# Kernel tuning notes

Measured on AMD Instinct MI355X. Metric: run time of the kernel, lower is better.

The kernel has to match this reference:

```python
import jax, jax.numpy as jnp
import numpy as np

B, S, D, H, E, K = 2, 1024, 768, 12, 8, 2
DF = 4 * D
HD = D // H
EPS = 1e-5

def layer_norm(x, g, b):
    m = jnp.mean(x, axis=-1, keepdims=True)
    v = jnp.mean(jnp.square(x - m), axis=-1, keepdims=True)
    return (x - m) * jax.lax.rsqrt(v + EPS) * g + b

def setup_inputs() -> dict:
    key = jax.random.key(0)
    ks = jax.random.split(key, 16)
    s = lambda i, shape, sc: jax.random.normal(ks[i], shape, jnp.float32) * sc
    return {
        'x': s(0, (B, S, D), 1.0),
        'ln1_g': jnp.ones((D,), jnp.float32), 'ln1_b': jnp.zeros((D,), jnp.float32),
        'Wq': s(1, (D, D), 0.02), 'Wk': s(2, (D, D), 0.02), 'Wv': s(3, (D, D), 0.02),
        'Wo': s(4, (D, D), 0.02), 'bo': jnp.zeros((D,), jnp.float32),
        'ln2_g': jnp.ones((D,), jnp.float32), 'ln2_b': jnp.zeros((D,), jnp.float32),
        'Wr': s(5, (D, E), 0.02), 'br': jnp.zeros((E,), jnp.float32),
        'W1': s(6, (E, D, DF), 0.02), 'b1': jnp.zeros((E, DF), jnp.float32),
        'W2': s(7, (E, DF, D), 0.02), 'b2': jnp.zeros((E, D), jnp.float32),
    }

def _attn(xn, Wq, Wk, Wv, Wo, bo):
    # xn: [B,S,D]
    q = (xn @ Wq).reshape(B, S, H, HD).transpose(0, 2, 1, 3)
    k = (xn @ Wk).reshape(B, S, H, HD).transpose(0, 2, 1, 3)
    v = (xn @ Wv).reshape(B, S, H, HD).transpose(0, 2, 1, 3)
    scores = jnp.einsum('bhqd,bhkd->bhqk', q, k) / jnp.sqrt(jnp.float32(HD))
    causal = jnp.tril(jnp.ones((S, S), bool))
    scores = jnp.where(causal, scores, jnp.float32(-1e9))
    w = jax.nn.softmax(scores, axis=-1)
    out = jnp.einsum('bhqk,bhkd->bhqd', w, v)
    out = out.transpose(0, 2, 1, 3).reshape(B, S, D)
    return out @ Wo + bo

def _smoe(xn, Wr, br, W1, b1, W2, b2):
    logits = xn @ Wr + br                               # [B,S,E]
    topv, topi = jax.lax.top_k(logits, K)               # [B,S,K]
    gw = jax.nn.softmax(topv, axis=-1)                  # softmax over selected experts
    oh = jax.nn.one_hot(topi, E, dtype=xn.dtype)        # [B,S,K,E]
    gate = jnp.einsum('bske,bsk->bse', oh, gw)          # sparse gate, zeros elsewhere
    h = jax.nn.gelu(jnp.einsum('bsd,edf->bsef', xn, W1) + b1, approximate=False)
    eo = jnp.einsum('bsef,efd->bsed', h, W2) + b2       # [B,S,E,D]
    return jnp.einsum('bsed,bse->bsd', eo, gate)

def reference(x, ln1_g, ln1_b, Wq, Wk, Wv, Wo, bo, ln2_g, ln2_b, Wr, br, W1, b1, W2, b2):
    h = x + _attn(layer_norm(x, ln1_g, ln1_b), Wq, Wk, Wv, Wo, bo)
    out = h + _smoe(layer_norm(h, ln2_g, ln2_b), Wr, br, W1, b1, W2, b2)
    return out
```

## Files before the change

### kernel.cpp

```cpp
#include <hip/hip_runtime.h>

using bf16x8 = __attribute__((ext_vector_type(8))) short;
using f32x4  = __attribute__((ext_vector_type(4))) float;

#define DEV __device__ __forceinline__

DEV short f2bf(float x){
  unsigned u = __float_as_uint(x);
  u += 0x7fffu + ((u >> 16) & 1u);
  return (short)(u >> 16);
}
DEV float bf2f(short h){ return __uint_as_float(((unsigned)(unsigned short)h) << 16); }

#define MFMA16(a,b,c) __builtin_amdgcn_mfma_f32_16x16x32_bf16(a,b,c,0,0,0)

DEV void gl_lds16(const void* g, void* l){
  __builtin_amdgcn_global_load_lds(
      (const __attribute__((address_space(1))) unsigned*)g,
      (__attribute__((address_space(3))) unsigned*)l, 16, 0, 0);
}


__global__ void k_transpose(const float* __restrict__ src, long sbatch,
                            short* __restrict__ dhi, short* __restrict__ dlo, long dbatch,
                            int R, int C){
  __shared__ float tile[32][33];
  const float* s = src + (long)blockIdx.z * sbatch;
  int c0 = blockIdx.x * 32, r0 = blockIdx.y * 32;
  int tx = threadIdx.x & 31, ty = threadIdx.x >> 5;
  #pragma unroll
  for (int i = 0; i < 4; i++)
    tile[ty + 8*i][tx] = s[(long)(r0 + ty + 8*i) * C + c0 + tx];
  __syncthreads();
  #pragma unroll
  for (int i = 0; i < 4; i++){
    int c = c0 + ty + 8*i;
    float v = tile[tx][ty + 8*i];
    short hv = f2bf(v);
    long o = (long)blockIdx.z * dbatch + (long)c * R + r0 + tx;
    dhi[o] = hv;
    if (dlo) dlo[o] = f2bf(v - bf2f(hv));
  }
}

__global__ void k_ln1(const float* __restrict__ x, const float* __restrict__ g,
                      const float* __restrict__ bb,
                      short* __restrict__ xh, short* __restrict__ xl){
  int t = blockIdx.x, tid = threadIdx.x;
  const float* xr = x + (long)t * 768;
  float v[3];
  #pragma unroll
  for (int j = 0; j < 3; j++) v[j] = xr[tid + 256*j];
  float s = v[0]+v[1]+v[2];
  float q = v[0]*v[0]+v[1]*v[1]+v[2]*v[2];
  #pragma unroll
  for (int o = 32; o > 0; o >>= 1){ s += __shfl_down(s,o,64); q += __shfl_down(q,o,64); }
  __shared__ float ss[4], qs[4];
  int w = tid >> 6;
  if ((tid & 63) == 0){ ss[w] = s; qs[w] = q; }
  __syncthreads();
  float St = ss[0]+ss[1]+ss[2]+ss[3], Qt = qs[0]+qs[1]+qs[2]+qs[3];
  float mean = St * (1.f/768.f);
  float var  = Qt * (1.f/768.f) - mean*mean;
  float inv  = 1.f / sqrtf(var + 1e-5f);
  #pragma unroll
  for (int j = 0; j < 3; j++){
    int d = tid + 256*j;
    float xn = (v[j]-mean)*inv*g[d] + bb[d];
    short hv = f2bf(xn);
    xh[(long)t*768 + d] = hv;
    xl[(long)t*768 + d] = f2bf(xn - bf2f(hv));
  }
}

__global__ __launch_bounds__(256,2) void k_qkv(
    const short* __restrict__ Ah, const short* __restrict__ Al,
    const short* __restrict__ Bh, const short* __restrict__ Bl,
    short* __restrict__ qh, short* __restrict__ ql,
    short* __restrict__ kh, short* __restrict__ kl,
    short* __restrict__ vh, short* __restrict__ vl){
  int M0 = blockIdx.x * 128, N0 = blockIdx.y * 128;
  __shared__ __align__(16) short lah[128*32], lal[128*32], lbh[128*32], lbl[128*32];
  int tid = threadIdx.x;
  int w = tid >> 6, lane = tid & 63, l15 = lane & 15, quad = lane >> 4;
  int mbase = (w & 1) * 64, nbase = (w >> 1) * 64;
  f32x4 acc[4][4];
  #pragma unroll
  for (int i = 0; i < 4; i++)
    #pragma unroll
    for (int j = 0; j < 4; j++) acc[i][j] = (f32x4){0.f,0.f,0.f,0.f};
  int sr = w*32 + (lane >> 2);
  int sc = ((lane & 3) ^ (sr & 3)) * 8;
  long gA = (long)(M0 + sr)*768 + sc;
  long gB = (long)(N0 + sr)*768 + sc;
  int swq = (quad ^ (l15 & 3)) * 8;
  for (int k0 = 0; k0 < 768; k0 += 32){
    gl_lds16(Ah + gA + k0,          lah + w*1024);
    gl_lds16(Ah + gA + 16*768 + k0, lah + w*1024 + 512);
    gl_lds16(Al + gA + k0,          lal + w*1024);
    gl_lds16(Al + gA + 16*768 + k0, lal + w*1024 + 512);
    gl_lds16(Bh + gB + k0,          lbh + w*1024);
    gl_lds16(Bh + gB + 16*768 + k0, lbh + w*1024 + 512);
    gl_lds16(Bl + gB + k0,          lbl + w*1024);
    gl_lds16(Bl + gB + 16*768 + k0, lbl + w*1024 + 512);
    __syncthreads();
    bf16x8 afh[4], afl[4];
    #pragma unroll
    for (int mt = 0; mt < 4; mt++){
      afh[mt] = *(const bf16x8*)&lah[(mbase+mt*16+l15)*32 + swq];
      afl[mt] = *(const bf16x8*)&lal[(mbase+mt*16+l15)*32 + swq];
    }
    #pragma unroll
    for (int nt = 0; nt < 4; nt++){
      bf16x8 bfh = *(const bf16x8*)&lbh[(nbase+nt*16+l15)*32 + swq];
      bf16x8 bfl = *(const bf16x8*)&lbl[(nbase+nt*16+l15)*32 + swq];
      #pragma unroll
      for (int mt = 0; mt < 4; mt++){
        acc[mt][nt] = MFMA16(afh[mt], bfh, acc[mt][nt]);
        acc[mt][nt] = MFMA16(afh[mt], bfl, acc[mt][nt]);
        acc[mt][nt] = MFMA16(afl[mt], bfh, acc[mt][nt]);
      }
    }
    __syncthreads();
  }
  #pragma unroll
  for (int mt = 0; mt < 4; mt++){
    #pragma unroll
    for (int nt = 0; nt < 4; nt++){
      #pragma unroll
      for (int rg = 0; rg < 4; rg++){
        int m = M0 + mbase + mt*16 + quad*4 + rg;
        int n = N0 + nbase + nt*16 + l15;
        float vv = acc[mt][nt][rg];
        int bi = m >> 10, si = m & 1023;
        if (n < 768){
          float sv = vv * 0.125f;
          short hv = f2bf(sv);
          int hh = n >> 6, hd = n & 63;
          long o = (((long)(bi*12+hh)*1024) + si)*64 + hd;
          qh[o] = hv; ql[o] = f2bf(sv - bf2f(hv));
        } else if (n < 1536){
          int n2 = n - 768;
          short hv = f2bf(vv);
          int hh = n2 >> 6, hd = n2 & 63;
          long o = (((long)(bi*12+hh)*1024) + si)*64 + hd;
          kh[o] = hv; kl[o] = f2bf(vv - bf2f(hv));
        } else {
          int n2 = n - 1536;
          short hv = f2bf(vv);
          int hh = n2 >> 6, hd = n2 & 63;
          long o = (((long)(bi*12+hh)*64) + hd)*1024 + si;
          vh[o] = hv; vl[o] = f2bf(vv - bf2f(hv));
        }
      }
    }
  }
}

__global__ __launch_bounds__(256,3) void k_attn(
    const short* __restrict__ qh, const short* __restrict__ ql,
    const short* __restrict__ kh, const short* __restrict__ kl,
    const short* __restrict__ vth, const short* __restrict__ vtl,
    float* __restrict__ po, float* __restrict__ pm, float* __restrict__ pl){
  int qt = blockIdx.x >> 1, half = blockIdx.x & 1, bh = blockIdx.y;
  int q0 = qt * 64;
  long base = (long)bh * 1024 * 64;
  int ktb = half ? ((qt + 2) >> 1) : 0;
  int kte = half ? (qt + 1) : ((qt + 2) >> 1);
  __shared__ __align__(16) short skh[64*64], skl[64*64], svh[64*64], svl[64*64];
  __shared__ __align__(16) short sph[4][16*72], spl[4][16*72];
  int tid = threadIdx.x, w = tid >> 6, lane = tid & 63, l15 = lane & 15, quad = lane >> 4;
  bf16x8 qfh[2], qfl[2];
  #pragma unroll
  for (int c = 0; c < 2; c++){
    long qa = base + (long)(q0 + w*16 + l15)*64 + c*32 + quad*8;
    qfh[c] = *(const bf16x8*)(qh + qa);
    qfl[c] = *(const bf16x8*)(ql + qa);
  }
  f32x4 oacc[4];
  #pragma unroll
  for (int i = 0; i < 4; i++) oacc[i] = (f32x4){0.f,0.f,0.f,0.f};
  float m_i[4] = {-1e30f,-1e30f,-1e30f,-1e30f};
  float l_i[4] = {0.f,0.f,0.f,0.f};
  const short* gsrc = (w==0) ? kh : (w==1) ? kl : (w==2) ? vth : vtl;
  short* myb = (w==0) ? skh : (w==1) ? skl : (w==2) ? svh : svl;
  bool isv = (w >= 2);
  int rloc = lane >> 3, pch = lane & 7;
  for (int kt = ktb; kt < kte; kt++){
    #pragma unroll
    for (int j = 0; j < 8; j++){
      int r = j*8 + rloc;
      int c = pch ^ (r & 7);
      long ga = isv ? (base + (long)r*1024 + kt*64 + c*8)
                    : (base + (long)(kt*64 + r)*64 + c*8);
      gl_lds16(gsrc + ga, myb + j*512);
    }
    __syncthreads();
    f32x4 sfr[4];
    #pragma unroll
    for (int nt = 0; nt < 4; nt++){
      f32x4 c = (f32x4){0.f,0.f,0.f,0.f};
      int krow = (nt*16 + l15) * 64;
      #pragma unroll
      for (int ch = 0; ch < 2; ch++){
        int pc = ((ch*4 + quad) ^ (l15 & 7)) * 8;
        bf16x8 kfh = *(const bf16x8*)&skh[krow + pc];
        bf16x8 kfl = *(const bf16x8*)&skl[krow + pc];
        c = MFMA16(qfh[ch], kfh, c);
        c = MFMA16(qfh[ch], kfl, c);
        c = MFMA16(qfl[ch], kfh, c);
      }
      sfr[nt] = c;
    }
    if (kt == qt){
      #pragma unroll
      for (int nt = 0; nt < 4; nt++)
        #pragma unroll
        for (int rg = 0; rg < 4; rg++){
          int kp = nt*16 + l15, qp = w*16 + quad*4 + rg;
          if (kp > qp) sfr[nt][rg] = -1e30f;
        }
    }
    float rmax[4];
    #pragma unroll
    for (int rg = 0; rg < 4; rg++)
      rmax[rg] = fmaxf(fmaxf(sfr[0][rg], sfr[1][rg]), fmaxf(sfr[2][rg], sfr[3][rg]));
    #pragma unroll
    for (int xm = 1; xm < 16; xm <<= 1)
      #pragma unroll
      for (int rg = 0; rg < 4; rg++)
        rmax[rg] = fmaxf(rmax[rg], __shfl_xor(rmax[rg], xm, 64));
    float alpha[4];
    #pragma unroll
    for (int rg = 0; rg < 4; rg++){
      float mn = fmaxf(m_i[rg], rmax[rg]);
      alpha[rg] = expf(m_i[rg] - mn);
      m_i[rg] = mn;
    }
    float rsum[4] = {0.f,0.f,0.f,0.f};
    #pragma unroll
    for (int nt = 0; nt < 4; nt++)
      #pragma unroll
      for (int rg = 0; rg < 4; rg++){
        float p = expf(sfr[nt][rg] - m_i[rg]);
        sfr[nt][rg] = p; rsum[rg] += p;
      }
    #pragma unroll
    for (int xm = 1; xm < 16; xm <<= 1)
      #pragma unroll
      for (int rg = 0; rg < 4; rg++)
        rsum[rg] += __shfl_xor(rsum[rg], xm, 64);
    #pragma unroll
    for (int rg = 0; rg < 4; rg++) l_i[rg] = l_i[rg]*alpha[rg] + rsum[rg];
    #pragma unroll
    for (int hd = 0; hd < 4; hd++)
      #pragma unroll
      for (int rg = 0; rg < 4; rg++) oacc[hd][rg] *= alpha[rg];
    #pragma unroll
    for (int nt = 0; nt < 4; nt++)
      #pragma unroll
      for (int rg = 0; rg < 4; rg++){
        float p = sfr[nt][rg];
        short hv = f2bf(p);
        sph[w][(quad*4+rg)*72 + nt*16 + l15] = hv;
        spl[w][(quad*4+rg)*72 + nt*16 + l15] = f2bf(p - bf2f(hv));
      }
    bf16x8 pfh[2], pfl[2];
    #pragma unroll
    for (int ch = 0; ch < 2; ch++){
      pfh[ch] = *(const bf16x8*)&sph[w][l15*72 + ch*32 + quad*8];
      pfl[ch] = *(const bf16x8*)&spl[w][l15*72 + ch*32 + quad*8];
    }
    #pragma unroll
    for (int hd = 0; hd < 4; hd++){
      int vrow = (hd*16 + l15) * 64;
      #pragma unroll
      for (int ch = 0; ch < 2; ch++){
        int pc = ((ch*4 + quad) ^ (l15 & 7)) * 8;
        bf16x8 vfh = *(const bf16x8*)&svh[vrow + pc];
        bf16x8 vfl = *(const bf16x8*)&svl[vrow + pc];
        oacc[hd] = MFMA16(pfh[ch], vfh, oacc[hd]);
        oacc[hd] = MFMA16(pfh[ch], vfl, oacc[hd]);
        oacc[hd] = MFMA16(pfl[ch], vfh, oacc[hd]);
      }
    }
    __syncthreads();
  }
  long pb = ((long)(half*24 + bh)*1024);
  #pragma unroll
  for (int hdt = 0; hdt < 4; hdt++)
    #pragma unroll
    for (int rg = 0; rg < 4; rg++){
      int qp = q0 + w*16 + quad*4 + rg;
      po[(pb + qp)*64 + hdt*16 + l15] = oacc[hdt][rg];
    }
  if (l15 == 0){
    #pragma unroll
    for (int rg = 0; rg < 4; rg++){
      int qp = q0 + w*16 + quad*4 + rg;
      pm[pb + qp] = m_i[rg];
      pl[pb + qp] = l_i[rg];
    }
  }
}

__global__ void k_attn_combine(const float* __restrict__ po, const float* __restrict__ pm,
                               const float* __restrict__ pl,
                               short* __restrict__ oh, short* __restrict__ ol){
  int bh = blockIdx.y, tid = threadIdx.x;
  int r = blockIdx.x*64 + (tid >> 2);
  int c0 = (tid & 3) * 16;
  long i0 = (long)bh*1024 + r;
  long i1 = (long)(24 + bh)*1024 + r;
  float m0 = pm[i0], m1 = pm[i1], l0 = pl[i0], l1 = pl[i1];
  float m = fmaxf(m0, m1);
  float a0 = expf(m0 - m), a1 = expf(m1 - m);
  float inv = 1.f / (a0*l0 + a1*l1);
  a0 *= inv; a1 *= inv;
  int b = bh / 12, hh = bh % 12;
  long ob = ((long)(b*1024 + r))*768 + hh*64 + c0;
  short hv[16], lv[16];
  #pragma unroll
  for (int j = 0; j < 4; j++){
    float4 o0 = *(const float4*)&po[i0*64 + c0 + j*4];
    float4 o1 = *(const float4*)&po[i1*64 + c0 + j*4];
    float vs[4] = {a0*o0.x + a1*o1.x, a0*o0.y + a1*o1.y,
                   a0*o0.z + a1*o1.z, a0*o0.w + a1*o1.w};
    #pragma unroll
    for (int q = 0; q < 4; q++){
      short h = f2bf(vs[q]);
      hv[j*4+q] = h; lv[j*4+q] = f2bf(vs[q] - bf2f(h));
    }
  }
  *(bf16x8*)(oh + ob)     = *(bf16x8*)&hv[0];
  *(bf16x8*)(oh + ob + 8) = *(bf16x8*)&hv[8];
  *(bf16x8*)(ol + ob)     = *(bf16x8*)&lv[0];
  *(bf16x8*)(ol + ob + 8) = *(bf16x8*)&lv[8];
}

__global__ __launch_bounds__(256,2) void k_wo(
    const short* __restrict__ Ah, const short* __restrict__ Al,
    const short* __restrict__ Bh, const short* __restrict__ Bl,
    const float* __restrict__ x, const float* __restrict__ bo,
    float* __restrict__ hout){
  int M0 = blockIdx.x * 128, N0 = blockIdx.y * 128;
  __shared__ __align__(16) short lah[128*32], lal[128*32], lbh[128*32], lbl[128*32];
  int tid = threadIdx.x;
  int w = tid >> 6, lane = tid & 63, l15 = lane & 15, quad = lane >> 4;
  int mbase = (w & 1) * 64, nbase = (w >> 1) * 64;
  f32x4 acc[4][4];
  #pragma unroll
  for (int i = 0; i < 4; i++)
    #pragma unroll
    for (int j = 0; j < 4; j++) acc[i][j] = (f32x4){0.f,0.f,0.f,0.f};
  int sr = w*32 + (lane >> 2);
  int sc = ((lane & 3) ^ (sr & 3)) * 8;
  long gA = (long)(M0 + sr)*768 + sc;
  long gB = (long)(N0 + sr)*768 + sc;
  int swq = (quad ^ (l15 & 3)) * 8;
  for (int k0 = 0; k0 < 768; k0 += 32){
    gl_lds16(Ah + gA + k0,          lah + w*1024);
    gl_lds16(Ah + gA + 16*768 + k0, lah + w*1024 + 512);
    gl_lds16(Al + gA + k0,          lal + w*1024);
    gl_lds16(Al + gA + 16*768 + k0, lal + w*1024 + 512);
    gl_lds16(Bh + gB + k0,          lbh + w*1024);
    gl_lds16(Bh + gB + 16*768 + k0, lbh + w*1024 + 512);
    gl_lds16(Bl + gB + k0,          lbl + w*1024);
    gl_lds16(Bl + gB + 16*768 + k0, lbl + w*1024 + 512);
    __syncthreads();
    bf16x8 afh[4], afl[4];
    #pragma unroll
    for (int mt = 0; mt < 4; mt++){
      afh[mt] = *(const bf16x8*)&lah[(mbase+mt*16+l15)*32 + swq];
      afl[mt] = *(const bf16x8*)&lal[(mbase+mt*16+l15)*32 + swq];
    }
    #pragma unroll
    for (int nt = 0; nt < 4; nt++){
      bf16x8 bfh = *(const bf16x8*)&lbh[(nbase+nt*16+l15)*32 + swq];
      bf16x8 bfl = *(const bf16x8*)&lbl[(nbase+nt*16+l15)*32 + swq];
      #pragma unroll
      for (int mt = 0; mt < 4; mt++){
        acc[mt][nt] = MFMA16(afh[mt], bfh, acc[mt][nt]);
        acc[mt][nt] = MFMA16(afh[mt], bfl, acc[mt][nt]);
        acc[mt][nt] = MFMA16(afl[mt], bfh, acc[mt][nt]);
      }
    }
    __syncthreads();
  }
  #pragma unroll
  for (int mt = 0; mt < 4; mt++)
    #pragma unroll
    for (int nt = 0; nt < 4; nt++)
      #pragma unroll
      for (int rg = 0; rg < 4; rg++){
        int m = M0 + mbase + mt*16 + quad*4 + rg;
        int n = N0 + nbase + nt*16 + l15;
        hout[(long)m*768 + n] = acc[mt][nt][rg] + x[(long)m*768 + n] + bo[n];
      }
}

__global__ void k_zero(int* cnt){ if (threadIdx.x < 8) cnt[threadIdx.x] = 0; }

__global__ void k_router(const float* __restrict__ h, const float* __restrict__ g,
                         const float* __restrict__ bb, const float* __restrict__ Wr,
                         const float* __restrict__ br, short* __restrict__ xn2,
                         int* __restrict__ cnt, int* __restrict__ perm,
                         float* __restrict__ gw){
  int t = blockIdx.x, tid = threadIdx.x;
  const float* xr = h + (long)t * 768;
  float v[3];
  #pragma unroll
  for (int j = 0; j < 3; j++) v[j] = xr[tid + 256*j];
  float s = v[0]+v[1]+v[2];
  float q = v[0]*v[0]+v[1]*v[1]+v[2]*v[2];
  #pragma unroll
  for (int o = 32; o > 0; o >>= 1){ s += __shfl_down(s,o,64); q += __shfl_down(q,o,64); }
  __shared__ float ss[4], qs[4];
  __shared__ float lred[4][8];
  int w = tid >> 6;
  if ((tid & 63) == 0){ ss[w] = s; qs[w] = q; }
  __syncthreads();
  float St = ss[0]+ss[1]+ss[2]+ss[3], Qt = qs[0]+qs[1]+qs[2]+qs[3];
  float mean = St * (1.f/768.f);
  float var  = Qt * (1.f/768.f) - mean*mean;
  float inv  = 1.f / sqrtf(var + 1e-5f);
  float part[8] = {0,0,0,0,0,0,0,0};
  #pragma unroll
  for (int j = 0; j < 3; j++){
    int d = tid + 256*j;
    float xn = (v[j]-mean)*inv*g[d] + bb[d];
    xn2[(long)t*768 + d] = f2bf(xn);
    #pragma unroll
    for (int e = 0; e < 8; e++) part[e] += xn * Wr[d*8 + e];
  }
  #pragma unroll
  for (int o = 32; o > 0; o >>= 1)
    #pragma unroll
    for (int e = 0; e < 8; e++) part[e] += __shfl_down(part[e], o, 64);
  if ((tid & 63) == 0)
    #pragma unroll
    for (int e = 0; e < 8; e++) lred[w][e] = part[e];
  __syncthreads();
  if (tid == 0){
    float lg[8];
    #pragma unroll
    for (int e = 0; e < 8; e++) lg[e] = lred[0][e]+lred[1][e]+lred[2][e]+lred[3][e] + br[e];
    int i1 = 0;
    for (int e = 1; e < 8; e++) if (lg[e] > lg[i1]) i1 = e;
    int i2 = -1;
    for (int e = 0; e < 8; e++){ if (e == i1) continue; if (i2 < 0 || lg[e] > lg[i2]) i2 = e; }
    float e2 = expf(lg[i2] - lg[i1]);
    float is = 1.f / (1.f + e2);
    gw[t*2]   = is;
    gw[t*2+1] = e2 * is;
    int p1 = atomicAdd(&cnt[i1], 1); perm[i1*2048 + p1] = t*2;
    int p2 = atomicAdd(&cnt[i2], 1); perm[i2*2048 + p2] = t*2 + 1;
  }
}

__global__ void k_scan(const int* __restrict__ cnt, int* __restrict__ poffs,
                       int* __restrict__ eidx, int* __restrict__ mbc,
                       int* __restrict__ ptot){
  if (threadIdx.x == 0){
    int p = 0;
    for (int e = 0; e < 8; e++){
      poffs[e] = p;
      int pc = (cnt[e] + 127) & ~127;
      mbc[e] = pc >> 7;
      for (int j = p >> 7; j < (p + pc) >> 7; j++) eidx[j] = e;
      p += pc;
    }
    *ptot = p;
    for (int j = p >> 7; j < 40; j++) eidx[j] = 7;
  }
}

__global__ void k_fill(const int* __restrict__ cnt, const int* __restrict__ poffs,
                       const int* __restrict__ eidx, const int* __restrict__ perm,
                       const int* __restrict__ ptot, int* __restrict__ pperm,
                       int* __restrict__ inv){
  int i = blockIdx.x*256 + threadIdx.x;
  int e = eidx[i >> 7];
  int li = i - poffs[e];
  int v = -1;
  if (i < *ptot && li >= 0 && li < cnt[e]){ v = perm[e*2048 + li]; inv[v] = i; }
  pperm[i] = v;
}

__global__ __launch_bounds__(256,3) void k_moe1(
    const short* __restrict__ xn2, const short* __restrict__ W1T,
    const float* __restrict__ b1,
    const int* __restrict__ poffs, const int* __restrict__ mbc,
    const int* __restrict__ pperm, short* __restrict__ h1){
  int t = blockIdx.x;
  int e = t / 24, n = t % 24;
  if ((int)blockIdx.y >= mbc[e]) return;
  int M0 = poffs[e] + blockIdx.y * 128;
  int N0 = n * 128;
  const short* Bp = W1T + (long)e * 3072 * 768;
  __shared__ __align__(16) short la[128*64], lb[128*64];
  __shared__ int rtok[128];
  int tid = threadIdx.x, w = tid >> 6, lane = tid & 63, l15 = lane & 15, quad = lane >> 4;
  if (tid < 128) rtok[tid] = pperm[M0 + tid];
  __syncthreads();
  int rl = lane >> 3, pch = lane & 7;
  long gA[4], gB[4];
  #pragma unroll
  for (int j = 0; j < 4; j++){
    int r = w*32 + j*8 + rl;
    int c = pch ^ (r & 7);
    int tk = rtok[r]; tk = (tk >= 0) ? (tk >> 1) : 0;
    gA[j] = (long)tk*768 + c*8;
    gB[j] = (long)(N0 + r)*768 + c*8;
  }
  short* ldA = la + w*2048;
  short* ldB = lb + w*2048;
  f32x4 acc[4][4];
  #pragma unroll
  for (int i = 0; i < 4; i++)
    #pragma unroll
    for (int j = 0; j < 4; j++) acc[i][j] = (f32x4){0.f,0.f,0.f,0.f};
  int mbase = (w & 1) * 64, nbase = (w >> 1) * 64;
  for (int k0 = 0; k0 < 768; k0 += 64){
    #pragma unroll
    for (int j = 0; j < 4; j++) gl_lds16(xn2 + gA[j] + k0, ldA + j*512);
    #pragma unroll
    for (int j = 0; j < 4; j++) gl_lds16(Bp  + gB[j] + k0, ldB + j*512);
    __syncthreads();
    #pragma unroll
    for (int kk = 0; kk < 2; kk++){
      int swq = ((kk*4 + quad) ^ (l15 & 7)) * 8;
      bf16x8 af[4];
      #pragma unroll
      for (int mt = 0; mt < 4; mt++)
        af[mt] = *(const bf16x8*)&la[(mbase+mt*16+l15)*64 + swq];
      #pragma unroll
      for (int nt = 0; nt < 4; nt++){
        bf16x8 bf = *(const bf16x8*)&lb[(nbase+nt*16+l15)*64 + swq];
        #pragma unroll
        for (int mt = 0; mt < 4; mt++) acc[mt][nt] = MFMA16(af[mt], bf, acc[mt][nt]);
      }
    }
    __syncthreads();
  }
  #pragma unroll
  for (int mt = 0; mt < 4; mt++)
    #pragma unroll
    for (int nt = 0; nt < 4; nt++)
      #pragma unroll
      for (int rg = 0; rg < 4; rg++){
        int ml = mbase + mt*16 + quad*4 + rg;
        if (rtok[ml] >= 0){
          int nn = N0 + nbase + nt*16 + l15;
          float vv = acc[mt][nt][rg] + b1[e*3072 + nn];
          float gl = 0.5f * vv * (1.f + erff(vv * 0.70710678118654752f));
          h1[(long)(M0 + ml)*3072 + nn] = f2bf(gl);
        }
      }
}

__global__ __launch_bounds__(256,3) void k_moe2(
    const short* __restrict__ h1, const short* __restrict__ W2T,
    const float* __restrict__ b2,
    const int* __restrict__ poffs, const int* __restrict__ mbc,
    float* __restrict__ e0, float* __restrict__ e1){
  int t = blockIdx.x;
  int e = t / 12, r12 = t % 12;
  int n = r12 >> 1, ks = r12 & 1;
  if ((int)blockIdx.y >= mbc[e]) return;
  int M0 = poffs[e] + blockIdx.y * 128;
  int N0 = n * 128;
  int kbeg = ks * 1536;
  const short* Bp = W2T + (long)e * 768 * 3072;
  float* eo = ks ? e1 : e0;
  __shared__ __align__(16) short la[128*64], lb[128*64];
  int tid = threadIdx.x, w = tid >> 6, lane = tid & 63, l15 = lane & 15, quad = lane >> 4;
  int rl = lane >> 3, pch = lane & 7;
  long gA[4], gB[4];
  #pragma unroll
  for (int j = 0; j < 4; j++){
    int r = w*32 + j*8 + rl;
    int c = pch ^ (r & 7);
    gA[j] = (long)(M0 + r)*3072 + kbeg + c*8;
    gB[j] = (long)(N0 + r)*3072 + kbeg + c*8;
  }
  short* ldA = la + w*2048;
  short* ldB = lb + w*2048;
  f32x4 acc[4][4];
  #pragma unroll
  for (int i = 0; i < 4; i++)
    #pragma unroll
    for (int j = 0; j < 4; j++) acc[i][j] = (f32x4){0.f,0.f,0.f,0.f};
  int mbase = (w & 1) * 64, nbase = (w >> 1) * 64;
  for (int k0 = 0; k0 < 1536; k0 += 64){
    #pragma unroll
    for (int j = 0; j < 4; j++) gl_lds16(h1 + gA[j] + k0, ldA + j*512);
    #pragma unroll
    for (int j = 0; j < 4; j++) gl_lds16(Bp + gB[j] + k0, ldB + j*512);
    __syncthreads();
    #pragma unroll
    for (int kk = 0; kk < 2; kk++){
      int swq = ((kk*4 + quad) ^ (l15 & 7)) * 8;
      bf16x8 af[4];
      #pragma unroll
      for (int mt = 0; mt < 4; mt++)
        af[mt] = *(const bf16x8*)&la[(mbase+mt*16+l15)*64 + swq];
      #pragma unroll
      for (int nt = 0; nt < 4; nt++){
        bf16x8 bf = *(const bf16x8*)&lb[(nbase+nt*16+l15)*64 + swq];
        #pragma unroll
        for (int mt = 0; mt < 4; mt++) acc[mt][nt] = MFMA16(af[mt], bf, acc[mt][nt]);
      }
    }
    __syncthreads();
  }
  #pragma unroll
  for (int mt = 0; mt < 4; mt++)
    #pragma unroll
    for (int nt = 0; nt < 4; nt++)
      #pragma unroll
      for (int rg = 0; rg < 4; rg++){
        int ml = mbase + mt*16 + quad*4 + rg;
        int nn = N0 + nbase + nt*16 + l15;
        float vv = acc[mt][nt][rg] + (ks ? 0.f : b2[e*768 + nn]);
        eo[(long)(M0 + ml)*768 + nn] = vv;
      }
}

__global__ void k_combine(const float* __restrict__ h,
                          const float* __restrict__ e0, const float* __restrict__ e1,
                          const int* __restrict__ inv, const float* __restrict__ gw,
                          float* __restrict__ out){
  int i = blockIdx.x * 256 + threadIdx.x;
  int t = i / 192, c = i - t * 192;
  int s0 = inv[2*t], s1 = inv[2*t+1];
  float g0 = gw[2*t], g1 = gw[2*t+1];
  float4 a  = ((const float4*)h)[i];
  float4 x0 = ((const float4*)e0)[(long)s0*192 + c];
  float4 y0 = ((const float4*)e1)[(long)s0*192 + c];
  float4 x1 = ((const float4*)e0)[(long)s1*192 + c];
  float4 y1 = ((const float4*)e1)[(long)s1*192 + c];
  float4 o;
  o.x = a.x + g0*(x0.x + y0.x) + g1*(x1.x + y1.x);
  o.y = a.y + g0*(x0.y + y0.y) + g1*(x1.y + y1.y);
  o.z = a.z + g0*(x0.z + y0.z) + g1*(x1.z + y1.z);
  o.w = a.w + g0*(x0.w + y0.w) + g1*(x1.w + y1.w);
  ((float4*)out)[i] = o;
}

extern "C" void kernel_launch(void* const* d_in, const int* in_sizes, int n_in,
                              void* d_out, int out_size, void* d_ws, size_t ws_size,
                              hipStream_t stream){
  const float* x    = (const float*)d_in[0];
  const float* ln1g = (const float*)d_in[1];
  const float* ln1b = (const float*)d_in[2];
  const float* Wq   = (const float*)d_in[3];
  const float* Wk   = (const float*)d_in[4];
  const float* Wv   = (const float*)d_in[5];
  const float* Wo   = (const float*)d_in[6];
  const float* bo   = (const float*)d_in[7];
  const float* ln2g = (const float*)d_in[8];
  const float* ln2b = (const float*)d_in[9];
  const float* Wr   = (const float*)d_in[10];
  const float* br   = (const float*)d_in[11];
  const float* W1   = (const float*)d_in[12];
  const float* b1   = (const float*)d_in[13];
  const float* W2   = (const float*)d_in[14];
  const float* b2   = (const float*)d_in[15];

  char* ws = (char*)d_ws;
  size_t off = 0;
  auto alloc = [&](size_t bytes) -> void* {
    void* p = ws + off;
    off += (bytes + 255) & ~(size_t)255;
    return p;
  };
  short* WQKVH = (short*)alloc(2304l*768*2);
  short* WQKVL = (short*)alloc(2304l*768*2);
  short* WOH   = (short*)alloc(768l*768*2);
  short* WOL   = (short*)alloc(768l*768*2);
  short* W1T   = (short*)alloc(8l*3072*768*2);
  short* W2T   = (short*)alloc(8l*768*3072*2);
  short* XN1H  = (short*)alloc(2048l*768*2);
  short* XN1L  = (short*)alloc(2048l*768*2);
  short* QH    = (short*)alloc(2048l*768*2);
  short* QL    = (short*)alloc(2048l*768*2);
  short* KH    = (short*)alloc(2048l*768*2);
  short* KL    = (short*)alloc(2048l*768*2);
  short* VTH   = (short*)alloc(2048l*768*2);
  short* VTL   = (short*)alloc(2048l*768*2);
  short* ATH   = (short*)alloc(2048l*768*2);
  short* ATL   = (short*)alloc(2048l*768*2);
  float* HBUF  = (float*)alloc(2048l*768*4);
  short* XN2   = (short*)alloc(2048l*768*2);
  short* H1    = (short*)alloc(5120l*3072*2);
  float* E0    = (float*)alloc(5120l*768*4);
  float* E1    = (float*)alloc(5120l*768*4);
  float* PO    = (float*)alloc(2l*24*1024*64*4);
  float* PM    = (float*)alloc(2l*24*1024*4);
  float* PL    = (float*)alloc(2l*24*1024*4);
  int*   CNT   = (int*)alloc(8*4);
  int*   POFF  = (int*)alloc(8*4);
  int*   EIDX  = (int*)alloc(40*4);
  int*   MBC   = (int*)alloc(8*4);
  int*   PTOT  = (int*)alloc(4);
  int*   PERM  = (int*)alloc(8l*2048*4);
  int*   PPERM = (int*)alloc(5120*4);
  int*   INV   = (int*)alloc(4096*4);
  float* GW    = (float*)alloc(4096*4);
  (void)ws_size; (void)in_sizes; (void)n_in; (void)out_size;

  k_transpose<<<dim3(24,24,1),256,0,stream>>>(Wq, 0, WQKVH,             WQKVL,             0, 768, 768);
  k_transpose<<<dim3(24,24,1),256,0,stream>>>(Wk, 0, WQKVH + 768l*768,  WQKVL + 768l*768,  0, 768, 768);
  k_transpose<<<dim3(24,24,1),256,0,stream>>>(Wv, 0, WQKVH + 1536l*768, WQKVL + 1536l*768, 0, 768, 768);
  k_transpose<<<dim3(24,24,1),256,0,stream>>>(Wo, 0, WOH, WOL, 0, 768, 768);
  k_transpose<<<dim3(96,24,8),256,0,stream>>>(W1, 768l*3072, W1T, nullptr, 3072l*768, 768, 3072);
  k_transpose<<<dim3(24,96,8),256,0,stream>>>(W2, 3072l*768, W2T, nullptr, 768l*3072, 3072, 768);

  k_ln1<<<2048,256,0,stream>>>(x, ln1g, ln1b, XN1H, XN1L);
  k_qkv<<<dim3(16,18),256,0,stream>>>(XN1H, XN1L, WQKVH, WQKVL, QH, QL, KH, KL, VTH, VTL);
  k_attn<<<dim3(32,24),256,0,stream>>>(QH, QL, KH, KL, VTH, VTL, PO, PM, PL);
  k_attn_combine<<<dim3(16,24),256,0,stream>>>(PO, PM, PL, ATH, ATL);
  k_wo<<<dim3(16,6),256,0,stream>>>(ATH, ATL, WOH, WOL, x, bo, HBUF);

  k_zero<<<1,64,0,stream>>>(CNT);
  k_router<<<2048,256,0,stream>>>(HBUF, ln2g, ln2b, Wr, br, XN2, CNT, PERM, GW);
  k_scan<<<1,64,0,stream>>>(CNT, POFF, EIDX, MBC, PTOT);
  k_fill<<<20,256,0,stream>>>(CNT, POFF, EIDX, PERM, PTOT, PPERM, INV);
  k_moe1<<<dim3(192,16),256,0,stream>>>(XN2, W1T, b1, POFF, MBC, PPERM, H1);
  k_moe2<<<dim3(96,16),256,0,stream>>>(H1, W2T, b2, POFF, MBC, E0, E1);
  k_combine<<<1536,256,0,stream>>>(HBUF, E0, E1, INV, GW, (float*)d_out);
}
```

Baseline: 511.8 us.

## Widen QKV/Wo GEMM K-tile to 64 and merge MoE routing kernels

The QKV and Wo GEMMs now stage 64-wide K slices in LDS with an 8-way XOR swizzle, which halves the number of barrier pairs per tile at the cost of doubling LDS per block (64 KB). The LayerNorm2 and router stage now processes two tokens per wavefront using only shuffle reductions and writes each token's selected experts to an array. A single 1024-thread block then computes the counts, offsets and permutation in shared memory, replacing the separate zero, scan and fill kernels. Fewer launches and global atomics are the goal. The trade-off is that the permutation order is no longer token-ordered, and the single build block runs serially.

```diff
diff --git a/kernel.cpp b/kernel.cpp
--- a/kernel.cpp
+++ b/kernel.cpp
@@ -80,7 +80,7 @@
     short* __restrict__ kh, short* __restrict__ kl,
     short* __restrict__ vh, short* __restrict__ vl){
   int M0 = blockIdx.x * 128, N0 = blockIdx.y * 128;
-  __shared__ __align__(16) short lah[128*32], lal[128*32], lbh[128*32], lbl[128*32];
+  __shared__ __align__(16) short lah[128*64], lal[128*64], lbh[128*64], lbl[128*64];
   int tid = threadIdx.x;
   int w = tid >> 6, lane = tid & 63, l15 = lane & 15, quad = lane >> 4;
   int mbase = (w & 1) * 64, nbase = (w >> 1) * 64;
@@ -89,36 +89,43 @@
   for (int i = 0; i < 4; i++)
     #pragma unroll
     for (int j = 0; j < 4; j++) acc[i][j] = (f32x4){0.f,0.f,0.f,0.f};
-  int sr = w*32 + (lane >> 2);
-  int sc = ((lane & 3) ^ (sr & 3)) * 8;
-  long gA = (long)(M0 + sr)*768 + sc;
-  long gB = (long)(N0 + sr)*768 + sc;
-  int swq = (quad ^ (l15 & 3)) * 8;
-  for (int k0 = 0; k0 < 768; k0 += 32){
-    gl_lds16(Ah + gA + k0,          lah + w*1024);
-    gl_lds16(Ah + gA + 16*768 + k0, lah + w*1024 + 512);
-    gl_lds16(Al + gA + k0,          lal + w*1024);
-    gl_lds16(Al + gA + 16*768 + k0, lal + w*1024 + 512);
-    gl_lds16(Bh + gB + k0,          lbh + w*1024);
-    gl_lds16(Bh + gB + 16*768 + k0, lbh + w*1024 + 512);
-    gl_lds16(Bl + gB + k0,          lbl + w*1024);
-    gl_lds16(Bl + gB + 16*768 + k0, lbl + w*1024 + 512);
-    __syncthreads();
-    bf16x8 afh[4], afl[4];
-    #pragma unroll
-    for (int mt = 0; mt < 4; mt++){
-      afh[mt] = *(const bf16x8*)&lah[(mbase+mt*16+l15)*32 + swq];
-      afl[mt] = *(const bf16x8*)&lal[(mbase+mt*16+l15)*32 + swq];
-    }
-    #pragma unroll
-    for (int nt = 0; nt < 4; nt++){
-      bf16x8 bfh = *(const bf16x8*)&lbh[(nbase+nt*16+l15)*32 + swq];
-      bf16x8 bfl = *(const bf16x8*)&lbl[(nbase+nt*16+l15)*32 + swq];
+  int rl = lane >> 3, pch = lane & 7;
+  long gA[4], gB[4];
+  #pragma unroll
+  for (int j = 0; j < 4; j++){
+    int r = w*32 + j*8 + rl;
+    int c = pch ^ (r & 7);
+    gA[j] = (long)(M0 + r)*768 + c*8;
+    gB[j] = (long)(N0 + r)*768 + c*8;
+  }
+  for (int k0 = 0; k0 < 768; k0 += 64){
+    #pragma unroll
+    for (int j = 0; j < 4; j++){
+      gl_lds16(Ah + gA[j] + k0, lah + w*2048 + j*512);
+      gl_lds16(Al + gA[j] + k0, lal + w*2048 + j*512);
+      gl_lds16(Bh + gB[j] + k0, lbh + w*2048 + j*512);
+      gl_lds16(Bl + gB[j] + k0, lbl + w*2048 + j*512);
+    }
+    __syncthreads();
+    #pragma unroll
+    for (int kk = 0; kk < 2; kk++){
+      int swq = ((kk*4 + quad) ^ (l15 & 7)) * 8;
+      bf16x8 afh[4], afl[4];
       #pragma unroll
       for (int mt = 0; mt < 4; mt++){
-        acc[mt][nt] = MFMA16(afh[mt], bfh, acc[mt][nt]);
-        acc[mt][nt] = MFMA16(afh[mt], bfl, acc[mt][nt]);
-        acc[mt][nt] = MFMA16(afl[mt], bfh, acc[mt][nt]);
+        afh[mt] = *(const bf16x8*)&lah[(mbase+mt*16+l15)*64 + swq];
+        afl[mt] = *(const bf16x8*)&lal[(mbase+mt*16+l15)*64 + swq];
+      }
+      #pragma unroll
+      for (int nt = 0; nt < 4; nt++){
+        bf16x8 bfh = *(const bf16x8*)&lbh[(nbase+nt*16+l15)*64 + swq];
+        bf16x8 bfl = *(const bf16x8*)&lbl[(nbase+nt*16+l15)*64 + swq];
+        #pragma unroll
+        for (int mt = 0; mt < 4; mt++){
+          acc[mt][nt] = MFMA16(afh[mt], bfh, acc[mt][nt]);
+          acc[mt][nt] = MFMA16(afh[mt], bfl, acc[mt][nt]);
+          acc[mt][nt] = MFMA16(afl[mt], bfh, acc[mt][nt]);
+        }
       }
     }
     __syncthreads();
@@ -344,7 +351,7 @@
     const float* __restrict__ x, const float* __restrict__ bo,
     float* __restrict__ hout){
   int M0 = blockIdx.x * 128, N0 = blockIdx.y * 128;
-  __shared__ __align__(16) short lah[128*32], lal[128*32], lbh[128*32], lbl[128*32];
+  __shared__ __align__(16) short lah[128*64], lal[128*64], lbh[128*64], lbl[128*64];
   int tid = threadIdx.x;
   int w = tid >> 6, lane = tid & 63, l15 = lane & 15, quad = lane >> 4;
   int mbase = (w & 1) * 64, nbase = (w >> 1) * 64;
@@ -353,36 +360,43 @@
   for (int i = 0; i < 4; i++)
     #pragma unroll
     for (int j = 0; j < 4; j++) acc[i][j] = (f32x4){0.f,0.f,0.f,0.f};
-  int sr = w*32 + (lane >> 2);
-  int sc = ((lane & 3) ^ (sr & 3)) * 8;
-  long gA = (long)(M0 + sr)*768 + sc;
-  long gB = (long)(N0 + sr)*768 + sc;
-  int swq = (quad ^ (l15 & 3)) * 8;
-  for (int k0 = 0; k0 < 768; k0 += 32){
-    gl_lds16(Ah + gA + k0,          lah + w*1024);
-    gl_lds16(Ah + gA + 16*768 + k0, lah + w*1024 + 512);
-    gl_lds16(Al + gA + k0,          lal + w*1024);
-    gl_lds16(Al + gA + 16*768 + k0, lal + w*1024 + 512);
-    gl_lds16(Bh + gB + k0,          lbh + w*1024);
-    gl_lds16(Bh + gB + 16*768 + k0, lbh + w*1024 + 512);
-    gl_lds16(Bl + gB + k0,          lbl + w*1024);
-    gl_lds16(Bl + gB + 16*768 + k0, lbl + w*1024 + 512);
-    __syncthreads();
-    bf16x8 afh[4], afl[4];
-    #pragma unroll
-    for (int mt = 0; mt < 4; mt++){
-      afh[mt] = *(const bf16x8*)&lah[(mbase+mt*16+l15)*32 + swq];
-      afl[mt] = *(const bf16x8*)&lal[(mbase+mt*16+l15)*32 + swq];
-    }
-    #pragma unroll
-    for (int nt = 0; nt < 4; nt++){
-      bf16x8 bfh = *(const bf16x8*)&lbh[(nbase+nt*16+l15)*32 + swq];
-      bf16x8 bfl = *(const bf16x8*)&lbl[(nbase+nt*16+l15)*32 + swq];
+  int rl = lane >> 3, pch = lane & 7;
+  long gA[4], gB[4];
+  #pragma unroll
+  for (int j = 0; j < 4; j++){
+    int r = w*32 + j*8 + rl;
+    int c = pch ^ (r & 7);
+    gA[j] = (long)(M0 + r)*768 + c*8;
+    gB[j] = (long)(N0 + r)*768 + c*8;
+  }
+  for (int k0 = 0; k0 < 768; k0 += 64){
+    #pragma unroll
+    for (int j = 0; j < 4; j++){
+      gl_lds16(Ah + gA[j] + k0, lah + w*2048 + j*512);
+      gl_lds16(Al + gA[j] + k0, lal + w*2048 + j*512);
+      gl_lds16(Bh + gB[j] + k0, lbh + w*2048 + j*512);
+      gl_lds16(Bl + gB[j] + k0, lbl + w*2048 + j*512);
+    }
+    __syncthreads();
+    #pragma unroll
+    for (int kk = 0; kk < 2; kk++){
+      int swq = ((kk*4 + quad) ^ (l15 & 7)) * 8;
+      bf16x8 afh[4], afl[4];
       #pragma unroll
       for (int mt = 0; mt < 4; mt++){
-        acc[mt][nt] = MFMA16(afh[mt], bfh, acc[mt][nt]);
-        acc[mt][nt] = MFMA16(afh[mt], bfl, acc[mt][nt]);
-        acc[mt][nt] = MFMA16(afl[mt], bfh, acc[mt][nt]);
+        afh[mt] = *(const bf16x8*)&lah[(mbase+mt*16+l15)*64 + swq];
+        afl[mt] = *(const bf16x8*)&lal[(mbase+mt*16+l15)*64 + swq];
+      }
+      #pragma unroll
+      for (int nt = 0; nt < 4; nt++){
+        bf16x8 bfh = *(const bf16x8*)&lbh[(nbase+nt*16+l15)*64 + swq];
+        bf16x8 bfl = *(const bf16x8*)&lbl[(nbase+nt*16+l15)*64 + swq];
+        #pragma unroll
+        for (int mt = 0; mt < 4; mt++){
+          acc[mt][nt] = MFMA16(afh[mt], bfh, acc[mt][nt]);
+          acc[mt][nt] = MFMA16(afh[mt], bfl, acc[mt][nt]);
+          acc[mt][nt] = MFMA16(afl[mt], bfh, acc[mt][nt]);
+        }
       }
     }
     __syncthreads();
@@ -399,92 +413,89 @@
       }
 }
 
-__global__ void k_zero(int* cnt){ if (threadIdx.x < 8) cnt[threadIdx.x] = 0; }
-
-__global__ void k_router(const float* __restrict__ h, const float* __restrict__ g,
-                         const float* __restrict__ bb, const float* __restrict__ Wr,
-                         const float* __restrict__ br, short* __restrict__ xn2,
-                         int* __restrict__ cnt, int* __restrict__ perm,
-                         float* __restrict__ gw){
-  int t = blockIdx.x, tid = threadIdx.x;
-  const float* xr = h + (long)t * 768;
-  float v[3];
-  #pragma unroll
-  for (int j = 0; j < 3; j++) v[j] = xr[tid + 256*j];
-  float s = v[0]+v[1]+v[2];
-  float q = v[0]*v[0]+v[1]*v[1]+v[2]*v[2];
-  #pragma unroll
-  for (int o = 32; o > 0; o >>= 1){ s += __shfl_down(s,o,64); q += __shfl_down(q,o,64); }
-  __shared__ float ss[4], qs[4];
-  __shared__ float lred[4][8];
-  int w = tid >> 6;
-  if ((tid & 63) == 0){ ss[w] = s; qs[w] = q; }
+__global__ void k_ln2router(const float* __restrict__ h, const float* __restrict__ g,
+                            const float* __restrict__ bb, const float* __restrict__ Wr,
+                            const float* __restrict__ br, short* __restrict__ xn2,
+                            int* __restrict__ sel, float* __restrict__ gw){
+  int wv = (blockIdx.x*256 + threadIdx.x) >> 6;
+  int lane = threadIdx.x & 63;
+  #pragma unroll
+  for (int rep = 0; rep < 2; rep++){
+    int t = wv*2 + rep;
+    const float* xr = h + (long)t * 768;
+    float v[12];
+    #pragma unroll
+    for (int j = 0; j < 12; j++) v[j] = xr[lane + 64*j];
+    float s = 0.f, q = 0.f;
+    #pragma unroll
+    for (int j = 0; j < 12; j++){ s += v[j]; q += v[j]*v[j]; }
+    #pragma unroll
+    for (int xm = 1; xm < 64; xm <<= 1){ s += __shfl_xor(s, xm, 64); q += __shfl_xor(q, xm, 64); }
+    float mean = s * (1.f/768.f);
+    float var  = q * (1.f/768.f) - mean*mean;
+    float inv  = 1.f / sqrtf(var + 1e-5f);
+    float part[8] = {0,0,0,0,0,0,0,0};
+    #pragma unroll
+    for (int j = 0; j < 12; j++){
+      int d = lane + 64*j;
+      float xn = (v[j]-mean)*inv*g[d] + bb[d];
+      xn2[(long)t*768 + d] = f2bf(xn);
+      #pragma unroll
+      for (int e = 0; e < 8; e++) part[e] += xn * Wr[d*8 + e];
+    }
+    #pragma unroll
+    for (int xm = 1; xm < 64; xm <<= 1)
+      #pragma unroll
+      for (int e = 0; e < 8; e++) part[e] += __shfl_xor(part[e], xm, 64);
+    if (lane == 0){
+      float lg[8];
+      #pragma unroll
+      for (int e = 0; e < 8; e++) lg[e] = part[e] + br[e];
+      int i1 = 0;
+      for (int e = 1; e < 8; e++) if (lg[e] > lg[i1]) i1 = e;
+      int i2 = -1;
+      for (int e = 0; e < 8; e++){ if (e == i1) continue; if (i2 < 0 || lg[e] > lg[i2]) i2 = e; }
+      float e2 = expf(lg[i2] - lg[i1]);
+      float is = 1.f / (1.f + e2);
+      gw[t*2]   = is;
+      gw[t*2+1] = e2 * is;
+      sel[t*2]   = i1;
+      sel[t*2+1] = i2;
+    }
+  }
+}
+
+__global__ void k_build(const int* __restrict__ sel, int* __restrict__ poffs,
+                        int* __restrict__ mbc, int* __restrict__ ptot,
+                        int* __restrict__ pperm, int* __restrict__ inv){
+  __shared__ int cnt8[8], cur[8];
+  int tid = threadIdx.x;
+  if (tid < 8) cnt8[tid] = 0;
   __syncthreads();
-  float St = ss[0]+ss[1]+ss[2]+ss[3], Qt = qs[0]+qs[1]+qs[2]+qs[3];
-  float mean = St * (1.f/768.f);
-  float var  = Qt * (1.f/768.f) - mean*mean;
-  float inv  = 1.f / sqrtf(var + 1e-5f);
-  float part[8] = {0,0,0,0,0,0,0,0};
-  #pragma unroll
-  for (int j = 0; j < 3; j++){
-    int d = tid + 256*j;
-    float xn = (v[j]-mean)*inv*g[d] + bb[d];
-    xn2[(long)t*768 + d] = f2bf(xn);
-    #pragma unroll
-    for (int e = 0; e < 8; e++) part[e] += xn * Wr[d*8 + e];
-  }
-  #pragma unroll
-  for (int o = 32; o > 0; o >>= 1)
-    #pragma unroll
-    for (int e = 0; e < 8; e++) part[e] += __shfl_down(part[e], o, 64);
-  if ((tid & 63) == 0)
-    #pragma unroll
-    for (int e = 0; e < 8; e++) lred[w][e] = part[e];
+  #pragma unroll
+  for (int r = 0; r < 4; r++) atomicAdd(&cnt8[sel[tid + r*1024]], 1);
   __syncthreads();
   if (tid == 0){
-    float lg[8];
-    #pragma unroll
-    for (int e = 0; e < 8; e++) lg[e] = lred[0][e]+lred[1][e]+lred[2][e]+lred[3][e] + br[e];
-    int i1 = 0;
-    for (int e = 1; e < 8; e++) if (lg[e] > lg[i1]) i1 = e;
-    int i2 = -1;
-    for (int e = 0; e < 8; e++){ if (e == i1) continue; if (i2 < 0 || lg[e] > lg[i2]) i2 = e; }
-    float e2 = expf(lg[i2] - lg[i1]);
-    float is = 1.f / (1.f + e2);
-    gw[t*2]   = is;
-    gw[t*2+1] = e2 * is;
-    int p1 = atomicAdd(&cnt[i1], 1); perm[i1*2048 + p1] = t*2;
-    int p2 = atomicAdd(&cnt[i2], 1); perm[i2*2048 + p2] = t*2 + 1;
-  }
-}
-
-__global__ void k_scan(const int* __restrict__ cnt, int* __restrict__ poffs,
-                       int* __restrict__ eidx, int* __restrict__ mbc,
-                       int* __restrict__ ptot){
-  if (threadIdx.x == 0){
     int p = 0;
     for (int e = 0; e < 8; e++){
-      poffs[e] = p;
-      int pc = (cnt[e] + 127) & ~127;
+      cur[e] = p; poffs[e] = p;
+      int pc = (cnt8[e] + 127) & ~127;
       mbc[e] = pc >> 7;
-      for (int j = p >> 7; j < (p + pc) >> 7; j++) eidx[j] = e;
       p += pc;
     }
     *ptot = p;
-    for (int j = p >> 7; j < 40; j++) eidx[j] = 7;
-  }
-}
-
-__global__ void k_fill(const int* __restrict__ cnt, const int* __restrict__ poffs,
-                       const int* __restrict__ eidx, const int* __restrict__ perm,
-                       const int* __restrict__ ptot, int* __restrict__ pperm,
-                       int* __restrict__ inv){
-  int i = blockIdx.x*256 + threadIdx.x;
-  int e = eidx[i >> 7];
-  int li = i - poffs[e];
-  int v = -1;
-  if (i < *ptot && li >= 0 && li < cnt[e]){ v = perm[e*2048 + li]; inv[v] = i; }
-  pperm[i] = v;
+  }
+  __syncthreads();
+  #pragma unroll
+  for (int r = 0; r < 5; r++) pperm[tid + r*1024] = -1;
+  __syncthreads();
+  #pragma unroll
+  for (int r = 0; r < 4; r++){
+    int i = tid + r*1024;
+    int pos = atomicAdd(&cur[sel[i]], 1);
+    pperm[pos] = i;
+    inv[i] = pos;
+  }
 }
 
 __global__ __launch_bounds__(256,3) void k_moe1(
@@ -699,12 +710,10 @@
   float* PO    = (float*)alloc(2l*24*1024*64*4);
   float* PM    = (float*)alloc(2l*24*1024*4);
   float* PL    = (float*)alloc(2l*24*1024*4);
-  int*   CNT   = (int*)alloc(8*4);
   int*   POFF  = (int*)alloc(8*4);
-  int*   EIDX  = (int*)alloc(40*4);
   int*   MBC   = (int*)alloc(8*4);
   int*   PTOT  = (int*)alloc(4);
-  int*   PERM  = (int*)alloc(8l*2048*4);
+  int*   SEL   = (int*)alloc(4096*4);
   int*   PPERM = (int*)alloc(5120*4);
   int*   INV   = (int*)alloc(4096*4);
   float* GW    = (float*)alloc(4096*4);
@@ -723,10 +732,8 @@
   k_attn_combine<<<dim3(16,24),256,0,stream>>>(PO, PM, PL, ATH, ATL);
   k_wo<<<dim3(16,6),256,0,stream>>>(ATH, ATL, WOH, WOL, x, bo, HBUF);
 
-  k_zero<<<1,64,0,stream>>>(CNT);
-  k_router<<<2048,256,0,stream>>>(HBUF, ln2g, ln2b, Wr, br, XN2, CNT, PERM, GW);
-  k_scan<<<1,64,0,stream>>>(CNT, POFF, EIDX, MBC, PTOT);
-  k_fill<<<20,256,0,stream>>>(CNT, POFF, EIDX, PERM, PTOT, PPERM, INV);
+  k_ln2router<<<256,256,0,stream>>>(HBUF, ln2g, ln2b, Wr, br, XN2, SEL, GW);
+  k_build<<<1,1024,0,stream>>>(SEL, POFF, MBC, PTOT, PPERM, INV);
   k_moe1<<<dim3(192,16),256,0,stream>>>(XN2, W1T, b1, POFF, MBC, PPERM, H1);
   k_moe2<<<dim3(96,16),256,0,stream>>>(H1, W2T, b2, POFF, MBC, E0, E1);
   k_combine<<<1536,256,0,stream>>>(HBUF, E0, E1, INV, GW, (float*)d_out);
```

New measurement: 467.8 us. -8.6%, faster.
